# Performance work log

Measured on AMD Instinct MI355X. Metric: run time of the kernel, lower is better.

The kernel has to match this reference:

```python
import jax, jax.numpy as jnp
import numpy as np

D_MODEL = 1024
NUM_HEADS = 16
DEPTH = D_MODEL // NUM_HEADS


def setup_inputs() -> dict:
    key = jax.random.key(0)
    ks = jax.random.split(key, 11)
    B, S, D = 2, 2048, D_MODEL
    s = 1.0 / np.sqrt(D)
    inp = {
        'x': jax.random.normal(ks[0], (B, S, D), jnp.float32),
        'pH': jax.random.normal(ks[1], (B, 1, 1), jnp.float32),
        'Wq': jax.random.normal(ks[2], (D, D), jnp.float32) * s,
        'bq': jnp.zeros((D,), jnp.float32),
        'Wk': jax.random.normal(ks[3], (D, D), jnp.float32) * s,
        'bk': jnp.zeros((D,), jnp.float32),
        'Wv': jax.random.normal(ks[4], (D, D), jnp.float32) * s,
        'bv': jnp.zeros((D,), jnp.float32),
        'Wo': jax.random.normal(ks[5], (D, D), jnp.float32) * s,
        'bo': jnp.zeros((D,), jnp.float32),
    }
    return inp


def reference(x, pH, Wq, bq, Wk, bk, Wv, bv, Wo, bo):
    B, S, D = x.shape
    H, dh = NUM_HEADS, DEPTH
    # QKV projections -> [B, H, S, dh]
    def proj(W, b):
        return (x @ W + b).reshape(B, S, H, dh).transpose(0, 2, 1, 3)
    q = proj(Wq, bq)
    k = proj(Wk, bk)
    v = proj(Wv, bv)
    # scores [B, H, S, S] with additive per-sample pH bias broadcast over heads/positions
    scores = jnp.einsum('bhqd,bhkd->bhqk', q, k) / jnp.sqrt(jnp.asarray(dh, x.dtype))
    scores = scores + pH[:, :, :, None]  # [B,1,1,1] broadcasts to [B,H,S,S]
    attn = jax.nn.softmax(scores, axis=-1)
    out = jnp.einsum('bhqk,bhkd->bhqd', attn, v)  # [B,H,S,dh]
    out = out.transpose(0, 2, 1, 3).reshape(B, S, D)
    return out @ Wo + bo  # dropout p=0.0 -> identity
```

## Files before the change

kernel.cpp:

```cpp
#include <hip/hip_runtime.h>
#include <hip/hip_bf16.h>
#include <math.h>

#define BATCH 2
#define SEQ   2048
#define DMODEL 1024
#define NHEADS 16
#define DHEAD 64
#define MROWS (BATCH*SEQ)

typedef __attribute__((ext_vector_type(8))) short bf16x8;
typedef __attribute__((ext_vector_type(4))) short bf16x4;
typedef __attribute__((ext_vector_type(4))) float f32x4;

__device__ __forceinline__ short f2bf(float f) {
    union { float f; unsigned u; } c; c.f = f;
    unsigned r = (c.u + 0x7fffu + ((c.u >> 16) & 1u)) >> 16;
    return (short)r;
}
__device__ __forceinline__ float bf2f(short h) {
    union { unsigned u; float f; } c; c.u = ((unsigned)(unsigned short)h) << 16;
    return c.f;
}

__device__ __forceinline__ void async_ld16(const void* g, void* l) {
    __builtin_amdgcn_global_load_lds(
        (const __attribute__((address_space(1))) unsigned*)g,
        (__attribute__((address_space(3))) unsigned*)l, 16, 0, 0);
}

__device__ __forceinline__ void pl32swap(unsigned &a, unsigned &b) {
    asm("v_permlane32_swap_b32 %0, %1" : "+v"(a), "+v"(b));
}
__device__ __forceinline__ void pl16swap(unsigned &a, unsigned &b) {
    asm("v_permlane16_swap_b32 %0, %1" : "+v"(a), "+v"(b));
}
__device__ __forceinline__ bf16x8 mk8(unsigned a, unsigned b, unsigned c, unsigned d) {
    union { unsigned u[4]; bf16x8 h; } t;
    t.u[0] = a; t.u[1] = b; t.u[2] = c; t.u[3] = d; return t.h;
}

__global__ __launch_bounds__(256) void prep(
    const float* __restrict__ x, short* __restrict__ xhi,
    const float* __restrict__ W0, const float* __restrict__ W1,
    const float* __restrict__ W2, const float* __restrict__ W3,
    short* __restrict__ oqkv, short* __restrict__ oo)
{
    __shared__ float T[64][65];
    const int tid = threadIdx.x;
    if (blockIdx.x < 2048) {
        const int i = blockIdx.x * 256 + tid;
        const float4* p = (const float4*)x + (size_t)i * 2;
        float4 a = p[0], b = p[1];
        float v[8] = {a.x, a.y, a.z, a.w, b.x, b.y, b.z, b.w};
        bf16x8 H;
        #pragma unroll
        for (int j = 0; j < 8; ++j) H[j] = f2bf(v[j]);
        *((bf16x8*)xhi + i) = H;
        return;
    }
    const int bi = blockIdx.x - 2048;
    const int z = bi >> 8;
    const int t = bi & 255;
    const float* W = (z == 0) ? W0 : (z == 1) ? W1 : (z == 2) ? W2 : W3;
    short* out = (z < 3) ? (oqkv + (size_t)z * 1024 * 1024) : oo;
    const int n0 = (t & 15) * 64, k0 = (t >> 4) * 64;
    #pragma unroll
    for (int i = 0; i < 16; ++i) {
        const int idx = tid + i * 256;
        const int r = idx >> 6, c = idx & 63;
        T[r][c] = W[(size_t)(k0 + r) * DMODEL + n0 + c];
    }
    __syncthreads();
    #pragma unroll
    for (int i = 0; i < 4; ++i) {
        const int idx = tid + i * 256;
        const int r = idx >> 4, g = idx & 15;
        bf16x4 H;
        #pragma unroll
        for (int j = 0; j < 4; ++j)
            H[j] = f2bf(T[g * 4 + j][r]);
        *(bf16x4*)(out + (size_t)(n0 + r) * DMODEL + k0 + g * 4) = H;
    }
}

__global__ __launch_bounds__(256, 3) void qkv_gemm(
    const short* __restrict__ Ahi, const short* __restrict__ Bthi,
    const float* __restrict__ b0, const float* __restrict__ b1, const float* __restrict__ b2,
    short* __restrict__ oqh, short* __restrict__ okh, short* __restrict__ ovh,
    float qscale)
{
    __shared__ short Ah[128 * 64], Bh[128 * 64];

    const int tid  = threadIdx.x;
    const int lane = tid & 63;
    const int w    = tid >> 6;
    const int quad = lane >> 4;
    const int l15  = lane & 15;
    const int wr   = w >> 1, wc = w & 1;
    const int m0   = blockIdx.y * 128;
    const int n0   = blockIdx.x * 128;
    const int K    = DMODEL;

    f32x4 acc[4][4] = {};

    for (int k0 = 0; k0 < K; k0 += 64) {
        __syncthreads();
        #pragma unroll
        for (int j = 0; j < 8; ++j) {
            const int base = w * 512 + j * 64;
            const int c = base + lane;
            if (base < 1024) {
                const int row = c >> 3, pos = (c & 7) ^ (row & 7);
                async_ld16(Ahi + (size_t)(m0 + row) * K + k0 + pos * 8, Ah + base * 8);
            } else {
                const int cb = c - 1024;
                const int row = cb >> 3, pos = (cb & 7) ^ (row & 7);
                async_ld16(Bthi + (size_t)(n0 + row) * K + k0 + pos * 8, Bh + (base - 1024) * 8);
            }
        }
        __syncthreads();

        #pragma unroll
        for (int s = 0; s < 2; ++s) {
            bf16x8 afh[4], bfh[4];
            #pragma unroll
            for (int mi = 0; mi < 4; ++mi) {
                const int row = wr * 64 + mi * 16 + l15;
                const int pos = (s * 4 + quad) ^ (row & 7);
                afh[mi] = *(const bf16x8*)(Ah + row * 64 + pos * 8);
            }
            #pragma unroll
            for (int ni = 0; ni < 4; ++ni) {
                const int row = wc * 64 + ni * 16 + l15;
                const int pos = (s * 4 + quad) ^ (row & 7);
                bfh[ni] = *(const bf16x8*)(Bh + row * 64 + pos * 8);
            }
            #pragma unroll
            for (int mi = 0; mi < 4; ++mi)
                #pragma unroll
                for (int ni = 0; ni < 4; ++ni)
                    acc[mi][ni] = __builtin_amdgcn_mfma_f32_16x16x32_bf16(
                        afh[mi], bfh[ni], acc[mi][ni], 0, 0, 0);
        }
    }

    const int nbase = n0 + wc * 64;
    const int which = nbase >> 10;
    const int hh = (nbase & 1023) >> 6;
    const int mb = m0 + wr * 64;
    const int b = mb >> 11, sbase = mb & (SEQ - 1);
    __syncthreads();
    short* scr = (w < 2) ? (Ah + w * 4096) : (Bh + (w - 2) * 4096);

    if (which < 2) {
        const float* bias = which ? b1 : b0;
        short* dstp = which ? okh : oqh;
        const float scl = which ? 1.0f : qscale;
        #pragma unroll
        for (int mi = 0; mi < 4; ++mi)
            #pragma unroll
            for (int ni = 0; ni < 4; ++ni)
                #pragma unroll
                for (int r = 0; r < 4; ++r) {
                    const int sloc = mi * 16 + quad * 4 + r;
                    const int dloc = ni * 16 + l15;
                    const int nn = (nbase + ni * 16 + l15) & 1023;
                    scr[sloc * 64 + (((dloc >> 3) ^ (sloc & 7)) * 8) + (dloc & 7)] =
                        f2bf((acc[mi][ni][r] + bias[nn]) * scl);
                }
        #pragma unroll
        for (int i = 0; i < 8; ++i) {
            const int sloc = i * 8 + (lane >> 3);
            const int cph = (lane & 7) ^ (sloc & 7);
            bf16x8 row = *(const bf16x8*)(scr + sloc * 64 + cph * 8);
            const int dloc = (lane & 7) * 8;
            *(bf16x8*)(dstp + ((size_t)(b * NHEADS + hh) * SEQ + sbase + sloc) * DHEAD + dloc) = row;
        }
    } else {
        #pragma unroll
        for (int mi = 0; mi < 4; ++mi)
            #pragma unroll
            for (int ni = 0; ni < 4; ++ni)
                #pragma unroll
                for (int r = 0; r < 4; ++r) {
                    const int sloc = mi * 16 + quad * 4 + r;
                    const int dloc = ni * 16 + l15;
                    const int nn = (nbase + ni * 16 + l15) & 1023;
                    scr[dloc * 64 + (((sloc >> 3) ^ (dloc & 7)) * 8) + (sloc & 7)] =
                        f2bf(acc[mi][ni][r] + b2[nn]);
                }
        #pragma unroll
        for (int i = 0; i < 8; ++i) {
            const int dloc = i * 8 + (lane >> 3);
            const int cph = (lane & 7) ^ (dloc & 7);
            bf16x8 row = *(const bf16x8*)(scr + dloc * 64 + cph * 8);
            const int sg = sbase + (lane & 7) * 8;
            *(bf16x8*)(ovh + ((size_t)(b * NHEADS + hh) * DHEAD + dloc) * SEQ + sg) = row;
        }
    }
}

__global__ __launch_bounds__(256) void ogemm(
    const short* __restrict__ Ahi, const short* __restrict__ Bthi,
    const float* __restrict__ b0, float* __restrict__ outf)
{
    __shared__ short Ah[64 * 64], Bh[128 * 64];

    const int tid  = threadIdx.x;
    const int lane = tid & 63;
    const int w    = tid >> 6;
    const int quad = lane >> 4;
    const int l15  = lane & 15;
    const int wr   = w >> 1, wc = w & 1;
    const int m0   = blockIdx.y * 64;
    const int n0   = blockIdx.x * 128;
    const int K    = DMODEL;

    f32x4 acc[2][4] = {};

    for (int k0 = 0; k0 < K; k0 += 64) {
        __syncthreads();
        #pragma unroll
        for (int j = 0; j < 6; ++j) {
            const int base = w * 384 + j * 64;
            const int c = base + lane;
            if (base < 512) {
                const int row = c >> 3, pos = (c & 7) ^ (row & 7);
                async_ld16(Ahi + (size_t)(m0 + row) * K + k0 + pos * 8, Ah + base * 8);
            } else {
                const int cb = c - 512;
                const int row = cb >> 3, pos = (cb & 7) ^ (row & 7);
                async_ld16(Bthi + (size_t)(n0 + row) * K + k0 + pos * 8, Bh + (base - 512) * 8);
            }
        }
        __syncthreads();

        #pragma unroll
        for (int s = 0; s < 2; ++s) {
            bf16x8 afh[2], bfh[4];
            #pragma unroll
            for (int mi = 0; mi < 2; ++mi) {
                const int row = wr * 32 + mi * 16 + l15;
                const int pos = (s * 4 + quad) ^ (row & 7);
                afh[mi] = *(const bf16x8*)(Ah + row * 64 + pos * 8);
            }
            #pragma unroll
            for (int ni = 0; ni < 4; ++ni) {
                const int row = wc * 64 + ni * 16 + l15;
                const int pos = (s * 4 + quad) ^ (row & 7);
                bfh[ni] = *(const bf16x8*)(Bh + row * 64 + pos * 8);
            }
            #pragma unroll
            for (int mi = 0; mi < 2; ++mi)
                #pragma unroll
                for (int ni = 0; ni < 4; ++ni)
                    acc[mi][ni] = __builtin_amdgcn_mfma_f32_16x16x32_bf16(
                        afh[mi], bfh[ni], acc[mi][ni], 0, 0, 0);
        }
    }

    #pragma unroll
    for (int mi = 0; mi < 2; ++mi)
        #pragma unroll
        for (int ni = 0; ni < 4; ++ni)
            #pragma unroll
            for (int r = 0; r < 4; ++r) {
                const int m = m0 + wr * 32 + mi * 16 + quad * 4 + r;
                const int nn = n0 + wc * 64 + ni * 16 + l15;
                outf[(size_t)m * DMODEL + nn] = acc[mi][ni][r] + b0[nn];
            }
}

__global__ __launch_bounds__(512) void attn_mfma(
    const short* __restrict__ Qh_g, const short* __restrict__ Kh_g,
    const short* __restrict__ Vth_g,
    short* __restrict__ op0, float* __restrict__ l0g)
{
    __shared__ short Ksh[4096];
    __shared__ short Vsh[4096];

    const int tid  = threadIdx.x;
    const int lane = tid & 63;
    const int w    = tid >> 6;
    const int quad = lane >> 4;
    const int l15  = lane & 15;

    const int bh    = blockIdx.x & 31;
    const int sk    = (blockIdx.x >> 5) & 3;
    const int qtile = blockIdx.x >> 7;
    const int q0    = qtile * 256 + w * 32;
    const size_t kvb = (size_t)bh * SEQ * DHEAD;

    bf16x8 ones;
    #pragma unroll
    for (int j = 0; j < 8; ++j) ones[j] = (short)0x3f80;

    bf16x8 qA[2], qB[2];
    {
        const size_t qrA = kvb + (size_t)(q0 + l15) * DHEAD;
        const size_t qrB = kvb + (size_t)(q0 + 16 + l15) * DHEAD;
        qA[0] = *(const bf16x8*)(Qh_g + qrA + quad * 8);
        qA[1] = *(const bf16x8*)(Qh_g + qrA + 32 + quad * 8);
        qB[0] = *(const bf16x8*)(Qh_g + qrB + quad * 8);
        qB[1] = *(const bf16x8*)(Qh_g + qrB + 32 + quad * 8);
    }

    const bool stager = (w < 4);
    const bool isv = (w >= 2) && stager;
    short* dst = isv ? Vsh : Ksh;
    int goff[4]; short* ldst[4];
    #pragma unroll
    for (int j = 0; j < 4; ++j) {
        const int c = (w & 1) * 256 + j * 64 + lane;
        const int row = c >> 3, pos = (c & 7) ^ (row & 7);
        goff[j] = isv ? (row * SEQ + pos * 8) : (row * DHEAD + pos * 8);
        ldst[j] = dst + (size_t)c * 8;
    }

    const int kb0 = sk * (SEQ / 4), kb1 = kb0 + SEQ / 4;
    const int step = isv ? 64 : 64 * DHEAD;
    const short* src = isv ? (Vth_g + kvb + kb0) : (Kh_g + kvb + (size_t)kb0 * DHEAD);

    f32x4 oA[4] = {}, oB[4] = {};
    f32x4 lAv = {}, lBv = {};

    bf16x8 stg[4];
    if (stager) {
        #pragma unroll
        for (int j = 0; j < 4; ++j) stg[j] = *(const bf16x8*)(src + goff[j]);
        src += step;
    }

    for (int kb = kb0; kb < kb1; kb += 64) {
        __syncthreads();
        if (stager) {
            #pragma unroll
            for (int j = 0; j < 4; ++j) *(bf16x8*)ldst[j] = stg[j];
        }
        __syncthreads();
        if (stager && kb + 64 < kb1) {
            #pragma unroll
            for (int j = 0; j < 4; ++j) stg[j] = *(const bf16x8*)(src + goff[j]);
            src += step;
        }

        unsigned pa[8], pb[8];
        #pragma unroll
        for (int mf = 0; mf < 4; ++mf) {
            const int row = mf * 16 + l15;
            const int sw = row & 7;
            bf16x8 kh0 = *(const bf16x8*)(Ksh + row * 64 + ((quad ^ sw) * 8));
            bf16x8 kh1 = *(const bf16x8*)(Ksh + row * 64 + (((4 + quad) ^ sw) * 8));
            f32x4 cA = {}, cB = {};
            cA = __builtin_amdgcn_mfma_f32_16x16x32_bf16(kh0, qA[0], cA, 0, 0, 0);
            cA = __builtin_amdgcn_mfma_f32_16x16x32_bf16(kh1, qA[1], cA, 0, 0, 0);
            cB = __builtin_amdgcn_mfma_f32_16x16x32_bf16(kh0, qB[0], cB, 0, 0, 0);
            cB = __builtin_amdgcn_mfma_f32_16x16x32_bf16(kh1, qB[1], cB, 0, 0, 0);

            unsigned uA[4], uB[4];
            #pragma unroll
            for (int r = 0; r < 4; ++r) {
                union { float f; unsigned u; } p;
                p.f = __builtin_amdgcn_exp2f(cA[r]);
                uA[r] = p.u;
                p.f = __builtin_amdgcn_exp2f(cB[r]);
                uB[r] = p.u;
            }
            pa[mf * 2]     = __builtin_amdgcn_perm(uA[1], uA[0], 0x07060302u);
            pa[mf * 2 + 1] = __builtin_amdgcn_perm(uA[3], uA[2], 0x07060302u);
            pb[mf * 2]     = __builtin_amdgcn_perm(uB[1], uB[0], 0x07060302u);
            pb[mf * 2 + 1] = __builtin_amdgcn_perm(uB[3], uB[2], 0x07060302u);
        }

        pl32swap(pa[0], pa[2]); pl32swap(pa[1], pa[3]);
        pl32swap(pa[4], pa[6]); pl32swap(pa[5], pa[7]);
        pl16swap(pa[0], pa[2]); pl16swap(pa[1], pa[3]);
        pl16swap(pa[4], pa[6]); pl16swap(pa[5], pa[7]);
        pl32swap(pb[0], pb[2]); pl32swap(pb[1], pb[3]);
        pl32swap(pb[4], pb[6]); pl32swap(pb[5], pb[7]);
        pl16swap(pb[0], pb[2]); pl16swap(pb[1], pb[3]);
        pl16swap(pb[4], pb[6]); pl16swap(pb[5], pb[7]);
        bf16x8 pA0 = mk8(pa[0], pa[1], pa[2], pa[3]);
        bf16x8 pA1 = mk8(pa[4], pa[5], pa[6], pa[7]);
        bf16x8 pB0 = mk8(pb[0], pb[1], pb[2], pb[3]);
        bf16x8 pB1 = mk8(pb[4], pb[5], pb[6], pb[7]);

        lAv = __builtin_amdgcn_mfma_f32_16x16x32_bf16(pA0, ones, lAv, 0, 0, 0);
        lAv = __builtin_amdgcn_mfma_f32_16x16x32_bf16(pA1, ones, lAv, 0, 0, 0);
        lBv = __builtin_amdgcn_mfma_f32_16x16x32_bf16(pB0, ones, lBv, 0, 0, 0);
        lBv = __builtin_amdgcn_mfma_f32_16x16x32_bf16(pB1, ones, lBv, 0, 0, 0);

        #pragma unroll
        for (int nf = 0; nf < 4; ++nf) {
            const int row = nf * 16 + l15;
            const int sw = row & 7;
            bf16x8 vh0 = *(const bf16x8*)(Vsh + row * 64 + ((quad ^ sw) * 8));
            bf16x8 vh1 = *(const bf16x8*)(Vsh + row * 64 + (((4 + quad) ^ sw) * 8));
            f32x4 cA = oA[nf], cB = oB[nf];
            cA = __builtin_amdgcn_mfma_f32_16x16x32_bf16(pA0, vh0, cA, 0, 0, 0);
            cA = __builtin_amdgcn_mfma_f32_16x16x32_bf16(pA1, vh1, cA, 0, 0, 0);
            cB = __builtin_amdgcn_mfma_f32_16x16x32_bf16(pB0, vh0, cB, 0, 0, 0);
            cB = __builtin_amdgcn_mfma_f32_16x16x32_bf16(pB1, vh1, cB, 0, 0, 0);
            oA[nf] = cA;
            oB[nf] = cB;
        }
    }

    short* op = op0 + (size_t)sk * 4194304;
    float* lg = l0g + sk * 65536;
    const int b = bh >> 4, hh = bh & 15;
    #pragma unroll
    for (int r = 0; r < 4; ++r) {
        const int qa = q0 + quad * 4 + r;
        if (l15 == 0) {
            lg[bh * SEQ + qa] = lAv[r];
            lg[bh * SEQ + qa + 16] = lBv[r];
        }
    }
    #pragma unroll
    for (int nf = 0; nf < 4; ++nf) {
        #pragma unroll
        for (int r = 0; r < 4; ++r) {
            const int qa = q0 + quad * 4 + r;
            const int d = nf * 16 + l15;
            op[(size_t)(b * SEQ + qa) * DMODEL + hh * DHEAD + d] = f2bf(oA[nf][r]);
            op[(size_t)(b * SEQ + qa + 16) * DMODEL + hh * DHEAD + d] = f2bf(oB[nf][r]);
        }
    }
}

__global__ __launch_bounds__(256) void combine_o(
    const short* __restrict__ op0, const float* __restrict__ l0g,
    short* __restrict__ aoh)
{
    const int i = blockIdx.x * 256 + threadIdx.x;
    const size_t e = (size_t)i * 8;
    const int qg = (int)(e >> 10);
    const int col = (int)(e & 1023);
    const int b = qg >> 11;
    const int q = qg & (SEQ - 1);
    const int bhq = (b * NHEADS + (col >> 6)) * SEQ + q;
    const float inv = 1.0f / (l0g[bhq] + l0g[bhq + 65536] +
                              l0g[bhq + 2 * 65536] + l0g[bhq + 3 * 65536]);

    bf16x8 a0 = *((const bf16x8*)op0 + i);
    bf16x8 a1 = *((const bf16x8*)(op0 + 4194304) + i);
    bf16x8 a2 = *((const bf16x8*)(op0 + 2 * 4194304) + i);
    bf16x8 a3 = *((const bf16x8*)(op0 + 3 * 4194304) + i);
    bf16x8 H;
    #pragma unroll
    for (int j = 0; j < 8; ++j)
        H[j] = f2bf((bf2f(a0[j]) + bf2f(a1[j]) + bf2f(a2[j]) + bf2f(a3[j])) * inv);
    *((bf16x8*)aoh + i) = H;
}

extern "C" void kernel_launch(void* const* d_in, const int* in_sizes, int n_in,
                              void* d_out, int out_size, void* d_ws, size_t ws_size,
                              hipStream_t stream) {
    const float* x  = (const float*)d_in[0];
    const float* Wq = (const float*)d_in[2];
    const float* bq = (const float*)d_in[3];
    const float* Wk = (const float*)d_in[4];
    const float* bk = (const float*)d_in[5];
    const float* Wv = (const float*)d_in[6];
    const float* bv = (const float*)d_in[7];
    const float* Wo = (const float*)d_in[8];
    const float* bo = (const float*)d_in[9];
    float* out = (float*)d_out;

    char* ws = (char*)d_ws;
    const size_t MB = 1024 * 1024;
    short* qh  = (short*)(ws + 0 * MB);
    short* kh  = (short*)(ws + 16 * MB);
    short* vth = (short*)(ws + 32 * MB);
    short* aoh = (short*)(ws + 48 * MB);
    short* op0 = (short*)(ws + 56 * MB);
    short* xhi = (short*)(ws + 64 * MB);
    short* wqkv_hi = (short*)(ws + 80 * MB);
    float* l0g = (float*)(ws + 88 * MB);
    short* wto_hi  = (short*)(ws + 92 * MB);

    dim3 blk(256);

    hipLaunchKernelGGL(prep, dim3(2048 + 1024), blk, 0, stream,
                       x, xhi, Wq, Wk, Wv, Wo, wqkv_hi, wto_hi);

    const float qscale = 0.125f * 1.44269504088896f;
    hipLaunchKernelGGL(qkv_gemm, dim3(3072 / 128, MROWS / 128), blk, 0, stream,
                       xhi, wqkv_hi, bq, bk, bv, qh, kh, vth, qscale);

    hipLaunchKernelGGL(attn_mfma, dim3(BATCH * NHEADS * (SEQ / 256) * 4), dim3(512), 0, stream,
                       qh, kh, vth, op0, l0g);

    hipLaunchKernelGGL(combine_o, dim3(MROWS * DMODEL / 8 / 256), blk, 0, stream,
                       op0, l0g, aoh);

    hipLaunchKernelGGL(ogemm, dim3(1024 / 128, MROWS / 64), blk, 0, stream,
                       aoh, wto_hi, bo, out);
}
```

Measured before the change: 186.4 us.

## Drop split-K attention and fuse normalization into attention kernel epilogue

Removes the 4-way split over the key dimension in the attention kernel, so each block now processes the full sequence and normalizes its output by the row sum directly. The separate combine kernel and the partial-output and partial-sum buffers are eliminated. This saves one launch plus the write and re-read of four partial outputs. In exchange the grid shrinks from 1024 to 256 blocks of 512 threads, which may underfill the GPU's compute units and lengthen each block's serial loop.

Result: faster. 179.5 us (-3.7%).

```diff
diff --git a/kernel.cpp b/kernel.cpp
--- a/kernel.cpp
+++ b/kernel.cpp
@@ -275,7 +275,7 @@
 __global__ __launch_bounds__(512) void attn_mfma(
     const short* __restrict__ Qh_g, const short* __restrict__ Kh_g,
     const short* __restrict__ Vth_g,
-    short* __restrict__ op0, float* __restrict__ l0g)
+    short* __restrict__ aoh)
 {
     __shared__ short Ksh[4096];
     __shared__ short Vsh[4096];
@@ -287,8 +287,7 @@
     const int l15  = lane & 15;
 
     const int bh    = blockIdx.x & 31;
-    const int sk    = (blockIdx.x >> 5) & 3;
-    const int qtile = blockIdx.x >> 7;
+    const int qtile = blockIdx.x >> 5;
     const int q0    = qtile * 256 + w * 32;
     const size_t kvb = (size_t)bh * SEQ * DHEAD;
 
@@ -318,9 +317,9 @@
         ldst[j] = dst + (size_t)c * 8;
     }
 
-    const int kb0 = sk * (SEQ / 4), kb1 = kb0 + SEQ / 4;
+    const int kb1 = SEQ;
     const int step = isv ? 64 : 64 * DHEAD;
-    const short* src = isv ? (Vth_g + kvb + kb0) : (Kh_g + kvb + (size_t)kb0 * DHEAD);
+    const short* src = isv ? (Vth_g + kvb) : (Kh_g + kvb);
 
     f32x4 oA[4] = {}, oB[4] = {};
     f32x4 lAv = {}, lBv = {};
@@ -332,7 +331,7 @@
         src += step;
     }
 
-    for (int kb = kb0; kb < kb1; kb += 64) {
+    for (int kb = 0; kb < kb1; kb += 64) {
         __syncthreads();
         if (stager) {
             #pragma unroll
@@ -407,16 +406,12 @@
         }
     }
 
-    short* op = op0 + (size_t)sk * 4194304;
-    float* lg = l0g + sk * 65536;
     const int b = bh >> 4, hh = bh & 15;
+    f32x4 rA, rB;
     #pragma unroll
     for (int r = 0; r < 4; ++r) {
-        const int qa = q0 + quad * 4 + r;
-        if (l15 == 0) {
-            lg[bh * SEQ + qa] = lAv[r];
-            lg[bh * SEQ + qa + 16] = lBv[r];
-        }
+        rA[r] = 1.0f / lAv[r];
+        rB[r] = 1.0f / lBv[r];
     }
     #pragma unroll
     for (int nf = 0; nf < 4; ++nf) {
@@ -424,35 +419,10 @@
         for (int r = 0; r < 4; ++r) {
             const int qa = q0 + quad * 4 + r;
             const int d = nf * 16 + l15;
-            op[(size_t)(b * SEQ + qa) * DMODEL + hh * DHEAD + d] = f2bf(oA[nf][r]);
-            op[(size_t)(b * SEQ + qa + 16) * DMODEL + hh * DHEAD + d] = f2bf(oB[nf][r]);
-        }
-    }
-}
-
-__global__ __launch_bounds__(256) void combine_o(
-    const short* __restrict__ op0, const float* __restrict__ l0g,
-    short* __restrict__ aoh)
-{
-    const int i = blockIdx.x * 256 + threadIdx.x;
-    const size_t e = (size_t)i * 8;
-    const int qg = (int)(e >> 10);
-    const int col = (int)(e & 1023);
-    const int b = qg >> 11;
-    const int q = qg & (SEQ - 1);
-    const int bhq = (b * NHEADS + (col >> 6)) * SEQ + q;
-    const float inv = 1.0f / (l0g[bhq] + l0g[bhq + 65536] +
-                              l0g[bhq + 2 * 65536] + l0g[bhq + 3 * 65536]);
-
-    bf16x8 a0 = *((const bf16x8*)op0 + i);
-    bf16x8 a1 = *((const bf16x8*)(op0 + 4194304) + i);
-    bf16x8 a2 = *((const bf16x8*)(op0 + 2 * 4194304) + i);
-    bf16x8 a3 = *((const bf16x8*)(op0 + 3 * 4194304) + i);
-    bf16x8 H;
-    #pragma unroll
-    for (int j = 0; j < 8; ++j)
-        H[j] = f2bf((bf2f(a0[j]) + bf2f(a1[j]) + bf2f(a2[j]) + bf2f(a3[j])) * inv);
-    *((bf16x8*)aoh + i) = H;
+            aoh[(size_t)(b * SEQ + qa) * DMODEL + hh * DHEAD + d] = f2bf(oA[nf][r] * rA[r]);
+            aoh[(size_t)(b * SEQ + qa + 16) * DMODEL + hh * DHEAD + d] = f2bf(oB[nf][r] * rB[r]);
+        }
+    }
 }
 
 extern "C" void kernel_launch(void* const* d_in, const int* in_sizes, int n_in,
@@ -475,10 +445,8 @@
     short* kh  = (short*)(ws + 16 * MB);
     short* vth = (short*)(ws + 32 * MB);
     short* aoh = (short*)(ws + 48 * MB);
-    short* op0 = (short*)(ws + 56 * MB);
     short* xhi = (short*)(ws + 64 * MB);
     short* wqkv_hi = (short*)(ws + 80 * MB);
-    float* l0g = (float*)(ws + 88 * MB);
     short* wto_hi  = (short*)(ws + 92 * MB);
 
     dim3 blk(256);
@@ -490,11 +458,8 @@
     hipLaunchKernelGGL(qkv_gemm, dim3(3072 / 128, MROWS / 128), blk, 0, stream,
                        xhi, wqkv_hi, bq, bk, bv, qh, kh, vth, qscale);
 
-    hipLaunchKernelGGL(attn_mfma, dim3(BATCH * NHEADS * (SEQ / 256) * 4), dim3(512), 0, stream,
-                       qh, kh, vth, op0, l0g);
-
-    hipLaunchKernelGGL(combine_o, dim3(MROWS * DMODEL / 8 / 256), blk, 0, stream,
-                       op0, l0g, aoh);
+    hipLaunchKernelGGL(attn_mfma, dim3(BATCH * NHEADS * (SEQ / 256)), dim3(512), 0, stream,
+                       qh, kh, vth, aoh);
 
     hipLaunchKernelGGL(ogemm, dim3(1024 / 128, MROWS / 64), blk, 0, stream,
                        aoh, wto_hi, bo, out);
```
